# Kernel optimization log

Measured on AMD Instinct MI355X. Metric: run time of the kernel, lower is better.

The kernel has to match this reference:

```python
import jax, jax.numpy as jnp
import numpy as np

TOPK = 2
GATE_THRESHOLD = 0.5
GATE_ALPHA = 0.1
EPS = 1e-8


def setup_inputs() -> dict:
    key = jax.random.key(0)
    x = jax.random.normal(key, (8192, 1024), dtype=jnp.float32)
    return {"x": x}


def reference(x):
    B, D = x.shape
    # F.normalize(p=2, eps): x / max(||x||, eps)
    norm = jnp.linalg.norm(x, axis=-1, keepdims=True)
    xn = x / jnp.maximum(norm, EPS)

    # pairwise dots; diagonal (self) masked to -1; NN search is no_grad
    dots = jax.lax.stop_gradient(xn @ xn.T)  # [B, B]
    diag = jnp.arange(B)
    dots = dots.at[diag, diag].set(-1.0)
    _, idx = jax.lax.top_k(dots, TOPK)  # [B, TOPK]

    nn_vecs = xn[idx]  # [B, TOPK, D]
    # torch PairwiseDistance(2, eps): ||x1 - x2 + eps||_2
    diff = xn[:, None, :] - nn_vecs + EPS
    distances = jnp.sqrt(jnp.sum(diff * diff, axis=-1)).reshape(-1)  # [B*TOPK]
    losses = -jnp.log(distances + EPS)

    # gate enabled since gate_threshold > 0
    alpha = max(GATE_ALPHA, 1e-6)
    gate = jax.nn.sigmoid((losses - GATE_THRESHOLD) / alpha)
    lg = losses * gate
    weighted_mean = lg.mean()
    gated_mean = lg.sum() / jnp.maximum(gate.sum(), 1.0)
    return 0.5 * weighted_mean + 0.5 * gated_mean
```

## Files before the change

kernel.cpp:

```cpp
#include <hip/hip_runtime.h>
#include <math.h>

#define NROWS 8192
#define DIM   1024
#define NCHUNK 64
#define NTRI  2080

typedef __bf16 bf16x8 __attribute__((ext_vector_type(8)));
typedef float  f32x4  __attribute__((ext_vector_type(4)));

__device__ __forceinline__ unsigned short f2bf(float f) {
    unsigned int u = __float_as_uint(f);
    u = (u + 0x7FFFu + ((u >> 16) & 1u)) >> 16;
    return (unsigned short)u;
}

__device__ __forceinline__ void gld16(const void* g, void* l) {
    __builtin_amdgcn_global_load_lds(
        (__attribute__((address_space(1))) void*)g,
        (__attribute__((address_space(3))) void*)l,
        16, 0, 0);
}

template<int N>
__device__ __forceinline__ float dppror(float v) {
    return __int_as_float(__builtin_amdgcn_update_dpp(
        0, __float_as_int(v), 0x120 + N, 0xF, 0xF, false));
}

__device__ __forceinline__ void t2push(float& a1, float& a2, float v) {
    float hi = fmaxf(a1, v);
    float lo = fminf(a1, v);
    a1 = hi;
    a2 = fmaxf(a2, lo);
}

__device__ __forceinline__ void t2merge(float& a1, float& a2, float b1, float b2) {
    float hi = fmaxf(a1, b1);
    float lo = fminf(a1, b1);
    a1 = hi;
    a2 = fmaxf(fmaxf(a2, b2), lo);
}

__global__ __launch_bounds__(256) void knorm(const float* __restrict__ x,
                                             unsigned short* __restrict__ xn) {
    const int w = threadIdx.x >> 6, lane = threadIdx.x & 63;
    const int row = blockIdx.x * 4 + w;
    const float4* src = (const float4*)(x + (size_t)row * DIM);
    float4 v[4];
    float ss = 0.0f;
    #pragma unroll
    for (int i = 0; i < 4; i++) {
        v[i] = src[lane + 64 * i];
        ss += v[i].x * v[i].x + v[i].y * v[i].y + v[i].z * v[i].z + v[i].w * v[i].w;
    }
    #pragma unroll
    for (int d = 1; d < 64; d <<= 1) ss += __shfl_xor(ss, d);
    const float inv = 1.0f / fmaxf(sqrtf(ss), 1e-8f);
    unsigned short* dst = xn + (size_t)row * DIM;
    #pragma unroll
    for (int i = 0; i < 4; i++) {
        uint2 o;
        o.x = (unsigned)f2bf(v[i].x * inv) | ((unsigned)f2bf(v[i].y * inv) << 16);
        o.y = (unsigned)f2bf(v[i].z * inv) | ((unsigned)f2bf(v[i].w * inv) << 16);
        *(uint2*)(dst + (size_t)(lane + 64 * i) * 4) = o;
    }
}

__global__ __launch_bounds__(256) void kgram(const unsigned short* __restrict__ xn,
                                             float2* __restrict__ top2) {
    const int bid0 = blockIdx.x;
    const int bid = (bid0 & 7) * (NTRI / 8) + (bid0 >> 3);
    int by = (int)((sqrtf(8.0f * (float)bid + 1.0f) - 1.0f) * 0.5f);
    while ((by + 1) * (by + 2) / 2 <= bid) by++;
    while (by * (by + 1) / 2 > bid) by--;
    const int bx = bid - by * (by + 1) / 2;

    const int t = threadIdx.x;
    const int w = t >> 6, lane = t & 63;
    const int wr = w >> 1, wc = w & 1;
    const int g = lane >> 4, c = lane & 15;

    __shared__ __align__(16) unsigned short As[2][128 * 32];
    __shared__ __align__(16) unsigned short Bs[2][128 * 32];
    __shared__ float st2r[2][128][2];
    __shared__ float st2c[2][128][2];

    f32x4 acc[4][4];
    #pragma unroll
    for (int m = 0; m < 4; m++)
        #pragma unroll
        for (int n = 0; n < 4; n++) acc[m][n] = (f32x4)0.0f;

    const int rA0 = t >> 2, cp0 = (t & 3) * 8;
    const unsigned short* gA0 = xn + (size_t)(by * 128 + rA0) * DIM + cp0;
    const unsigned short* gA1 = gA0 + (size_t)64 * DIM;
    const unsigned short* gB0 = xn + (size_t)(bx * 128 + rA0) * DIM + cp0;
    const unsigned short* gB1 = gB0 + (size_t)64 * DIM;

    auto STAGE = [&](int buf, int kk) {
        gld16(gA0 + kk, (char*)&As[buf][0] + (size_t)w * 1024);
        gld16(gA1 + kk, (char*)&As[buf][0] + 4096 + (size_t)w * 1024);
        gld16(gB0 + kk, (char*)&Bs[buf][0] + (size_t)w * 1024);
        gld16(gB1 + kk, (char*)&Bs[buf][0] + 4096 + (size_t)w * 1024);
    };

    STAGE(0, 0);
    __syncthreads();

    int cur = 0;
    #pragma unroll 2
    for (int kk = 0; kk < DIM; kk += 32) {
        if (kk + 32 < DIM) STAGE(cur ^ 1, kk + 32);

        bf16x8 af[4], bf[4];
        #pragma unroll
        for (int m = 0; m < 4; m++)
            af[m] = *(const bf16x8*)(&As[cur][0] + (wr * 64 + m * 16 + c) * 32 + g * 8);
        #pragma unroll
        for (int n = 0; n < 4; n++)
            bf[n] = *(const bf16x8*)(&Bs[cur][0] + (wc * 64 + n * 16 + c) * 32 + g * 8);
        #pragma unroll
        for (int m = 0; m < 4; m++)
            #pragma unroll
            for (int n = 0; n < 4; n++)
                acc[m][n] = __builtin_amdgcn_mfma_f32_16x16x32_bf16(af[m], bf[n], acc[m][n], 0, 0, 0);

        __syncthreads();
        cur ^= 1;
    }

    const bool diagTile = (bx == by);

    #pragma unroll
    for (int m = 0; m < 4; m++) {
        #pragma unroll
        for (int r = 0; r < 4; r++) {
            const int lrow = wr * 64 + m * 16 + g * 4 + r;
            float a1 = -1e30f, a2 = -1e30f;
            #pragma unroll
            for (int n = 0; n < 4; n++) {
                float v = acc[m][n][r];
                if (diagTile && (wc * 64 + n * 16 + c) == lrow) v = -2.0f;
                t2push(a1, a2, v);
            }
            { float b1 = dppror<1>(a1), b2 = dppror<1>(a2); t2merge(a1, a2, b1, b2); }
            { float b1 = dppror<2>(a1), b2 = dppror<2>(a2); t2merge(a1, a2, b1, b2); }
            { float b1 = dppror<4>(a1), b2 = dppror<4>(a2); t2merge(a1, a2, b1, b2); }
            { float b1 = dppror<8>(a1), b2 = dppror<8>(a2); t2merge(a1, a2, b1, b2); }
            if (c == 0) { st2r[wc][lrow][0] = a1; st2r[wc][lrow][1] = a2; }
        }
    }

    if (!diagTile) {
        #pragma unroll
        for (int n = 0; n < 4; n++) {
            const int lcol = wc * 64 + n * 16 + c;
            float a1 = -1e30f, a2 = -1e30f;
            #pragma unroll
            for (int m = 0; m < 4; m++)
                #pragma unroll
                for (int r = 0; r < 4; r++)
                    t2push(a1, a2, acc[m][n][r]);
            #pragma unroll
            for (int d = 16; d < 64; d <<= 1) {
                float b1 = __shfl_xor(a1, d);
                float b2 = __shfl_xor(a2, d);
                t2merge(a1, a2, b1, b2);
            }
            if (g == 0) { st2c[wr][lcol][0] = a1; st2c[wr][lcol][1] = a2; }
        }
    }

    __syncthreads();
    if (t < 128) {
        float a1 = st2r[0][t][0], a2 = st2r[0][t][1];
        t2merge(a1, a2, st2r[1][t][0], st2r[1][t][1]);
        top2[(size_t)(by * 128 + t) * NCHUNK + bx] = make_float2(a1, a2);
    }
    if (!diagTile && t < 128) {
        float a1 = st2c[0][t][0], a2 = st2c[0][t][1];
        t2merge(a1, a2, st2c[1][t][0], st2c[1][t][1]);
        top2[(size_t)(bx * 128 + t) * NCHUNK + by] = make_float2(a1, a2);
    }
}

__global__ __launch_bounds__(256) void kloss(const float2* __restrict__ top2,
                                             float2* __restrict__ partials) {
    const int t = threadIdx.x;
    const int w = t >> 6, lane = t & 63;
    const int row = blockIdx.x * 4 + w;
    float2 q = top2[(size_t)row * NCHUNK + lane];
    float a1 = q.x, a2 = q.y;
    #pragma unroll
    for (int d = 1; d < 64; d <<= 1) {
        float b1 = __shfl_xor(a1, d);
        float b2 = __shfl_xor(a2, d);
        t2merge(a1, a2, b1, b2);
    }
    __shared__ float2 wsum[4];
    if (lane == 0) {
        float slg = 0.0f, sg = 0.0f;
        float vs[2] = {a1, a2};
        #pragma unroll
        for (int i = 0; i < 2; i++) {
            float dd = sqrtf(fmaxf(2.0f - 2.0f * vs[i], 0.0f));
            float loss = -logf(dd + 1e-8f);
            float gate = 1.0f / (1.0f + expf(-(loss - 0.5f) * 10.0f));
            slg += loss * gate;
            sg += gate;
        }
        wsum[w] = make_float2(slg, sg);
    }
    __syncthreads();
    if (t == 0) {
        float a = 0.0f, b = 0.0f;
        #pragma unroll
        for (int i = 0; i < 4; i++) { a += wsum[i].x; b += wsum[i].y; }
        partials[blockIdx.x] = make_float2(a, b);
    }
}

__global__ __launch_bounds__(256) void kfinal(const float2* __restrict__ partials,
                                              float* __restrict__ out) {
    const int t = threadIdx.x;
    float a = 0.0f, b = 0.0f;
    for (int i = t; i < 2048; i += 256) {
        float2 p = partials[i];
        a += p.x; b += p.y;
    }
    #pragma unroll
    for (int d = 1; d < 64; d <<= 1) {
        a += __shfl_xor(a, d);
        b += __shfl_xor(b, d);
    }
    __shared__ float2 ws4[4];
    if ((t & 63) == 0) ws4[t >> 6] = make_float2(a, b);
    __syncthreads();
    if (t == 0) {
        float A = 0.0f, Bb = 0.0f;
        #pragma unroll
        for (int i = 0; i < 4; i++) { A += ws4[i].x; Bb += ws4[i].y; }
        float wm = A / 16384.0f;
        float gm = A / fmaxf(Bb, 1.0f);
        out[0] = 0.5f * wm + 0.5f * gm;
    }
}

extern "C" void kernel_launch(void* const* d_in, const int* in_sizes, int n_in,
                              void* d_out, int out_size, void* d_ws, size_t ws_size,
                              hipStream_t stream) {
    const float* x = (const float*)d_in[0];
    unsigned short* xn = (unsigned short*)d_ws;
    float2* top2 = (float2*)((char*)d_ws + (size_t)16 * 1024 * 1024);
    float2* partials = (float2*)((char*)d_ws + (size_t)20 * 1024 * 1024);
    float* out = (float*)d_out;

    knorm<<<NROWS / 4, 256, 0, stream>>>(x, xn);
    kgram<<<NTRI, 256, 0, stream>>>(xn, top2);
    kloss<<<2048, 256, 0, stream>>>(top2, partials);
    kfinal<<<1, 256, 0, stream>>>(partials, out);
}
```

Measured before the change: 176.3 us.

## Enlarge gram tiles to 256x256 with triple-buffered swizzled LDS and persistent blocks

Moves the symmetric gram kernel from 128x128 tiles with 256 threads to 256x256 tiles with 512 threads, so each tile load is reused across more MFMA work. It adds a three-stage LDS pipeline with explicit vmcnt waits, an XOR-swizzled LDS layout to avoid bank conflicts, setprio around the MFMA bursts, and a persistent grid of 512 blocks that loops over 528 triangular tiles. kloss is adjusted for 32 column chunks. The cost is higher register and LDS use per block, which lowers occupancy, and a tail where a few blocks run a second tile.

After: 184.0 us. 1.04x slower.

```diff
diff --git a/kernel.cpp b/kernel.cpp
--- a/kernel.cpp
+++ b/kernel.cpp
@@ -3,8 +3,12 @@
 
 #define NROWS 8192
 #define DIM   1024
-#define NCHUNK 64
-#define NTRI  2080
+#define BT    256
+#define NCHUNK 32
+#define NTRI  528
+#define GRID  512
+#define NKT   32
+#define BK    32
 
 typedef __bf16 bf16x8 __attribute__((ext_vector_type(8)));
 typedef float  f32x4  __attribute__((ext_vector_type(4)));
@@ -67,121 +71,162 @@
     }
 }
 
-__global__ __launch_bounds__(256) void kgram(const unsigned short* __restrict__ xn,
+__global__ __launch_bounds__(512) void kgram(const unsigned short* __restrict__ xn,
                                              float2* __restrict__ top2) {
-    const int bid0 = blockIdx.x;
-    const int bid = (bid0 & 7) * (NTRI / 8) + (bid0 >> 3);
-    int by = (int)((sqrtf(8.0f * (float)bid + 1.0f) - 1.0f) * 0.5f);
-    while ((by + 1) * (by + 2) / 2 <= bid) by++;
-    while (by * (by + 1) / 2 > bid) by--;
-    const int bx = bid - by * (by + 1) / 2;
+    __shared__ __align__(16) char smem[110592];
+    float (*st2r)[256][2] = (float (*)[256][2])(smem + 98304);
+    float (*st2c)[256][2] = (float (*)[256][2])(smem + 98304 + 8192);
 
     const int t = threadIdx.x;
-    const int w = t >> 6, lane = t & 63;
-    const int wr = w >> 1, wc = w & 1;
+    const int lane = t & 63;
+    const int w = t >> 6;
+    const int wr = w >> 2, wc = w & 3;
     const int g = lane >> 4, c = lane & 15;
 
-    __shared__ __align__(16) unsigned short As[2][128 * 32];
-    __shared__ __align__(16) unsigned short Bs[2][128 * 32];
-    __shared__ float st2r[2][128][2];
-    __shared__ float st2c[2][128][2];
-
-    f32x4 acc[4][4];
-    #pragma unroll
-    for (int m = 0; m < 4; m++)
-        #pragma unroll
-        for (int n = 0; n < 4; n++) acc[m][n] = (f32x4)0.0f;
-
-    const int rA0 = t >> 2, cp0 = (t & 3) * 8;
-    const unsigned short* gA0 = xn + (size_t)(by * 128 + rA0) * DIM + cp0;
-    const unsigned short* gA1 = gA0 + (size_t)64 * DIM;
-    const unsigned short* gB0 = xn + (size_t)(bx * 128 + rA0) * DIM + cp0;
-    const unsigned short* gB1 = gB0 + (size_t)64 * DIM;
-
-    auto STAGE = [&](int buf, int kk) {
-        gld16(gA0 + kk, (char*)&As[buf][0] + (size_t)w * 1024);
-        gld16(gA1 + kk, (char*)&As[buf][0] + 4096 + (size_t)w * 1024);
-        gld16(gB0 + kk, (char*)&Bs[buf][0] + (size_t)w * 1024);
-        gld16(gB1 + kk, (char*)&Bs[buf][0] + 4096 + (size_t)w * 1024);
-    };
-
-    STAGE(0, 0);
-    __syncthreads();
-
-    int cur = 0;
-    #pragma unroll 2
-    for (int kk = 0; kk < DIM; kk += 32) {
-        if (kk + 32 < DIM) STAGE(cur ^ 1, kk + 32);
-
-        bf16x8 af[4], bf[4];
-        #pragma unroll
-        for (int m = 0; m < 4; m++)
-            af[m] = *(const bf16x8*)(&As[cur][0] + (wr * 64 + m * 16 + c) * 32 + g * 8);
-        #pragma unroll
-        for (int n = 0; n < 4; n++)
-            bf[n] = *(const bf16x8*)(&Bs[cur][0] + (wc * 64 + n * 16 + c) * 32 + g * 8);
-        #pragma unroll
-        for (int m = 0; m < 4; m++)
+    const int LA = c * 64 + (((g ^ (c & 3) ^ ((c >> 2) & 3)) & 3) << 4);
+
+    const int q0 = t, q1 = 512 + t;
+    const int r0 = q0 >> 2, g0 = (q0 & 3) ^ (r0 & 3) ^ ((r0 >> 2) & 3);
+    const int r1 = q1 >> 2, g1 = (q1 & 3) ^ (r1 & 3) ^ ((r1 >> 2) & 3);
+
+    const int bswz = (blockIdx.x & 7) * (GRID / 8) + (blockIdx.x >> 3);
+
+    for (int tix = bswz; tix < NTRI; tix += GRID) {
+        int by = (int)((sqrtf(8.0f * (float)tix + 1.0f) - 1.0f) * 0.5f);
+        while ((by + 1) * (by + 2) / 2 <= tix) by++;
+        while (by * (by + 1) / 2 > tix) by--;
+        const int bx = tix - by * (by + 1) / 2;
+        const bool diagTile = (bx == by);
+
+        const unsigned short* sA0 = xn + (size_t)(by * BT + r0) * DIM + g0 * 8;
+        const unsigned short* sA1 = xn + (size_t)(by * BT + r1) * DIM + g1 * 8;
+        const unsigned short* sB0 = xn + (size_t)(bx * BT + r0) * DIM + g0 * 8;
+        const unsigned short* sB1 = xn + (size_t)(bx * BT + r1) * DIM + g1 * 8;
+
+        f32x4 acc[8][4];
+        #pragma unroll
+        for (int m = 0; m < 8; m++)
             #pragma unroll
-            for (int n = 0; n < 4; n++)
-                acc[m][n] = __builtin_amdgcn_mfma_f32_16x16x32_bf16(af[m], bf[n], acc[m][n], 0, 0, 0);
-
-        __syncthreads();
-        cur ^= 1;
-    }
-
-    const bool diagTile = (bx == by);
-
-    #pragma unroll
-    for (int m = 0; m < 4; m++) {
-        #pragma unroll
-        for (int r = 0; r < 4; r++) {
-            const int lrow = wr * 64 + m * 16 + g * 4 + r;
-            float a1 = -1e30f, a2 = -1e30f;
+            for (int n = 0; n < 4; n++) acc[m][n] = (f32x4)0.0f;
+
+        auto STAGE = [&](int b, int kt) {
+            char* base = smem + b * 32768;
+            gld16(sA0 + kt * BK, base + q0 * 16);
+            gld16(sA1 + kt * BK, base + q1 * 16);
+            gld16(sB0 + kt * BK, base + 16384 + q0 * 16);
+            gld16(sB1 + kt * BK, base + 16384 + q1 * 16);
+        };
+
+        STAGE(0, 0);
+        STAGE(1, 1);
+        asm volatile("s_waitcnt vmcnt(4)" ::: "memory");
+        __builtin_amdgcn_s_barrier();
+        asm volatile("" ::: "memory");
+        __builtin_amdgcn_sched_barrier(0);
+
+        int cur = 0;
+        #pragma unroll 1
+        for (int kt = 0; kt < NKT; ++kt) {
+            if (kt + 2 < NKT) {
+                int nb = cur + 2; if (nb >= 3) nb -= 3;
+                STAGE(nb, kt + 2);
+            }
+            const char* Ab = smem + cur * 32768 + wr * 8192 + LA;
+            const char* Bb = smem + cur * 32768 + 16384 + wc * 4096 + LA;
+            bf16x8 b0 = *(const bf16x8*)(Bb + 0 * 1024);
+            bf16x8 b1 = *(const bf16x8*)(Bb + 1 * 1024);
+            bf16x8 b2 = *(const bf16x8*)(Bb + 2 * 1024);
+            bf16x8 b3 = *(const bf16x8*)(Bb + 3 * 1024);
+            #pragma unroll
+            for (int ph = 0; ph < 2; ++ph) {
+                bf16x8 a0 = *(const bf16x8*)(Ab + (ph * 4 + 0) * 1024);
+                bf16x8 a1 = *(const bf16x8*)(Ab + (ph * 4 + 1) * 1024);
+                bf16x8 a2 = *(const bf16x8*)(Ab + (ph * 4 + 2) * 1024);
+                bf16x8 a3 = *(const bf16x8*)(Ab + (ph * 4 + 3) * 1024);
+                asm volatile("s_waitcnt lgkmcnt(0)" ::: "memory");
+                __builtin_amdgcn_sched_barrier(0);
+                __builtin_amdgcn_s_setprio(1);
+                acc[ph*4+0][0] = __builtin_amdgcn_mfma_f32_16x16x32_bf16(a0, b0, acc[ph*4+0][0], 0, 0, 0);
+                acc[ph*4+0][1] = __builtin_amdgcn_mfma_f32_16x16x32_bf16(a0, b1, acc[ph*4+0][1], 0, 0, 0);
+                acc[ph*4+0][2] = __builtin_amdgcn_mfma_f32_16x16x32_bf16(a0, b2, acc[ph*4+0][2], 0, 0, 0);
+                acc[ph*4+0][3] = __builtin_amdgcn_mfma_f32_16x16x32_bf16(a0, b3, acc[ph*4+0][3], 0, 0, 0);
+                acc[ph*4+1][0] = __builtin_amdgcn_mfma_f32_16x16x32_bf16(a1, b0, acc[ph*4+1][0], 0, 0, 0);
+                acc[ph*4+1][1] = __builtin_amdgcn_mfma_f32_16x16x32_bf16(a1, b1, acc[ph*4+1][1], 0, 0, 0);
+                acc[ph*4+1][2] = __builtin_amdgcn_mfma_f32_16x16x32_bf16(a1, b2, acc[ph*4+1][2], 0, 0, 0);
+                acc[ph*4+1][3] = __builtin_amdgcn_mfma_f32_16x16x32_bf16(a1, b3, acc[ph*4+1][3], 0, 0, 0);
+                acc[ph*4+2][0] = __builtin_amdgcn_mfma_f32_16x16x32_bf16(a2, b0, acc[ph*4+2][0], 0, 0, 0);
+                acc[ph*4+2][1] = __builtin_amdgcn_mfma_f32_16x16x32_bf16(a2, b1, acc[ph*4+2][1], 0, 0, 0);
+                acc[ph*4+2][2] = __builtin_amdgcn_mfma_f32_16x16x32_bf16(a2, b2, acc[ph*4+2][2], 0, 0, 0);
+                acc[ph*4+2][3] = __builtin_amdgcn_mfma_f32_16x16x32_bf16(a2, b3, acc[ph*4+2][3], 0, 0, 0);
+                acc[ph*4+3][0] = __builtin_amdgcn_mfma_f32_16x16x32_bf16(a3, b0, acc[ph*4+3][0], 0, 0, 0);
+                acc[ph*4+3][1] = __builtin_amdgcn_mfma_f32_16x16x32_bf16(a3, b1, acc[ph*4+3][1], 0, 0, 0);
+                acc[ph*4+3][2] = __builtin_amdgcn_mfma_f32_16x16x32_bf16(a3, b2, acc[ph*4+3][2], 0, 0, 0);
+                acc[ph*4+3][3] = __builtin_amdgcn_mfma_f32_16x16x32_bf16(a3, b3, acc[ph*4+3][3], 0, 0, 0);
+                __builtin_amdgcn_s_setprio(0);
+                __builtin_amdgcn_sched_barrier(0);
+            }
+            if (kt + 1 < NKT) {
+                if (kt + 2 < NKT) asm volatile("s_waitcnt vmcnt(4)" ::: "memory");
+                else              asm volatile("s_waitcnt vmcnt(0)" ::: "memory");
+                __builtin_amdgcn_s_barrier();
+                asm volatile("" ::: "memory");
+                __builtin_amdgcn_sched_barrier(0);
+            }
+            cur = cur + 1; if (cur >= 3) cur -= 3;
+        }
+
+        #pragma unroll
+        for (int m = 0; m < 8; m++) {
+            #pragma unroll
+            for (int rr = 0; rr < 4; rr++) {
+                const int lrow = wr * 128 + m * 16 + g * 4 + rr;
+                float a1 = -1e30f, a2 = -1e30f;
+                #pragma unroll
+                for (int n = 0; n < 4; n++) {
+                    float v = acc[m][n][rr];
+                    if (diagTile && (wc * 64 + n * 16 + c) == lrow) v = -2.0f;
+                    t2push(a1, a2, v);
+                }
+                { float b1 = dppror<1>(a1), b2 = dppror<1>(a2); t2merge(a1, a2, b1, b2); }
+                { float b1 = dppror<2>(a1), b2 = dppror<2>(a2); t2merge(a1, a2, b1, b2); }
+                { float b1 = dppror<4>(a1), b2 = dppror<4>(a2); t2merge(a1, a2, b1, b2); }
+                { float b1 = dppror<8>(a1), b2 = dppror<8>(a2); t2merge(a1, a2, b1, b2); }
+                if (c == 0) { st2r[wc][lrow][0] = a1; st2r[wc][lrow][1] = a2; }
+            }
+        }
+        if (!diagTile) {
             #pragma unroll
             for (int n = 0; n < 4; n++) {
-                float v = acc[m][n][r];
-                if (diagTile && (wc * 64 + n * 16 + c) == lrow) v = -2.0f;
-                t2push(a1, a2, v);
-            }
-            { float b1 = dppror<1>(a1), b2 = dppror<1>(a2); t2merge(a1, a2, b1, b2); }
-            { float b1 = dppror<2>(a1), b2 = dppror<2>(a2); t2merge(a1, a2, b1, b2); }
-            { float b1 = dppror<4>(a1), b2 = dppror<4>(a2); t2merge(a1, a2, b1, b2); }
-            { float b1 = dppror<8>(a1), b2 = dppror<8>(a2); t2merge(a1, a2, b1, b2); }
-            if (c == 0) { st2r[wc][lrow][0] = a1; st2r[wc][lrow][1] = a2; }
-        }
-    }
-
-    if (!diagTile) {
-        #pragma unroll
-        for (int n = 0; n < 4; n++) {
-            const int lcol = wc * 64 + n * 16 + c;
-            float a1 = -1e30f, a2 = -1e30f;
-            #pragma unroll
-            for (int m = 0; m < 4; m++)
+                const int lcol = wc * 64 + n * 16 + c;
+                float a1 = -1e30f, a2 = -1e30f;
                 #pragma unroll
-                for (int r = 0; r < 4; r++)
-                    t2push(a1, a2, acc[m][n][r]);
-            #pragma unroll
-            for (int d = 16; d < 64; d <<= 1) {
-                float b1 = __shfl_xor(a1, d);
-                float b2 = __shfl_xor(a2, d);
-                t2merge(a1, a2, b1, b2);
-            }
-            if (g == 0) { st2c[wr][lcol][0] = a1; st2c[wr][lcol][1] = a2; }
-        }
-    }
-
-    __syncthreads();
-    if (t < 128) {
-        float a1 = st2r[0][t][0], a2 = st2r[0][t][1];
-        t2merge(a1, a2, st2r[1][t][0], st2r[1][t][1]);
-        top2[(size_t)(by * 128 + t) * NCHUNK + bx] = make_float2(a1, a2);
-    }
-    if (!diagTile && t < 128) {
-        float a1 = st2c[0][t][0], a2 = st2c[0][t][1];
-        t2merge(a1, a2, st2c[1][t][0], st2c[1][t][1]);
-        top2[(size_t)(bx * 128 + t) * NCHUNK + by] = make_float2(a1, a2);
+                for (int m = 0; m < 8; m++)
+                    #pragma unroll
+                    for (int rr = 0; rr < 4; rr++)
+                        t2push(a1, a2, acc[m][n][rr]);
+                #pragma unroll
+                for (int d = 16; d < 64; d <<= 1) {
+                    float b1 = __shfl_xor(a1, d);
+                    float b2 = __shfl_xor(a2, d);
+                    t2merge(a1, a2, b1, b2);
+                }
+                if (g == 0) { st2c[wr][lcol][0] = a1; st2c[wr][lcol][1] = a2; }
+            }
+        }
+        __syncthreads();
+        if (t < 256) {
+            float a1 = st2r[0][t][0], a2 = st2r[0][t][1];
+            t2merge(a1, a2, st2r[1][t][0], st2r[1][t][1]);
+            t2merge(a1, a2, st2r[2][t][0], st2r[2][t][1]);
+            t2merge(a1, a2, st2r[3][t][0], st2r[3][t][1]);
+            top2[(size_t)(by * BT + t) * NCHUNK + bx] = make_float2(a1, a2);
+        } else if (!diagTile) {
+            const int tc = t - 256;
+            float a1 = st2c[0][tc][0], a2 = st2c[0][tc][1];
+            t2merge(a1, a2, st2c[1][tc][0], st2c[1][tc][1]);
+            top2[(size_t)(bx * BT + tc) * NCHUNK + by] = make_float2(a1, a2);
+        }
+        __syncthreads();
     }
 }
 
@@ -190,8 +235,11 @@
     const int t = threadIdx.x;
     const int w = t >> 6, lane = t & 63;
     const int row = blockIdx.x * 4 + w;
-    float2 q = top2[(size_t)row * NCHUNK + lane];
-    float a1 = q.x, a2 = q.y;
+    float a1 = -1e30f, a2 = -1e30f;
+    if (lane < NCHUNK) {
+        float2 q = top2[(size_t)row * NCHUNK + lane];
+        a1 = q.x; a2 = q.y;
+    }
     #pragma unroll
     for (int d = 1; d < 64; d <<= 1) {
         float b1 = __shfl_xor(a1, d);
@@ -257,7 +305,7 @@
     float* out = (float*)d_out;
 
     knorm<<<NROWS / 4, 256, 0, stream>>>(x, xn);
-    kgram<<<NTRI, 256, 0, stream>>>(xn, top2);
+    kgram<<<GRID, 512, 0, stream>>>(xn, top2);
     kloss<<<2048, 256, 0, stream>>>(top2, partials);
     kfinal<<<1, 256, 0, stream>>>(partials, out);
 }
```
